# Optimization experiments

Hardware: AMD Instinct MI355X
Metric: run time of the kernel (lower is better)

## Reference

```python
import jax, jax.numpy as jnp
import numpy as np

CHANNEL = 16
KERNEL_SIZE = 5

def _gaussian3d_weight(channel, kernel_size):
    sigma = kernel_size / 6.0
    r = jnp.arange(-(kernel_size // 2), (kernel_size + 1) // 2, dtype=jnp.float32) ** 2
    # sum of squared offsets along each axis -> isotropic Gaussian
    k3 = r[None, None, :] + r[None, :, None] + r[:, None, None]
    k3 = jnp.exp(-k3 / (2.0 * sigma ** 2))
    k3 = k3 / k3.sum()
    # depthwise weight: [C_out=C, C_in/groups=1, kD, kH, kW]
    return jnp.broadcast_to(k3, (channel, 1, kernel_size, kernel_size, kernel_size))

def setup_inputs() -> dict:
    key = jax.random.key(0)
    x = jax.random.normal(key, (2, CHANNEL, 64, 128, 128), dtype=jnp.float32)
    weight = _gaussian3d_weight(CHANNEL, KERNEL_SIZE)
    return {"x": x, "weight": weight}

def reference(x, weight):
    # depthwise Conv3d, padding='same', groups=channel, no bias
    return jax.lax.conv_general_dilated(
        x, weight,
        window_strides=(1, 1, 1),
        padding='SAME',
        dimension_numbers=('NCDHW', 'OIDHW', 'NCDHW'),
        feature_group_count=CHANNEL,
    )
```

## Files before the change

### kernel.cpp

```cpp
#include <hip/hip_runtime.h>


#define DD 64
#define HH 128
#define WW 128
#define TH 8
#define NC 16
#define PITCH 136
#define RAWROWS 12
#define XOFF 4
#define ZCHUNK 32

__global__ __launch_bounds__(256, 4)
void gauss3d_sep_kernel(const float* __restrict__ x,
                        const float* __restrict__ wt,
                        float* __restrict__ out)
{
    __shared__ float raw[RAWROWS][PITCH];
    __shared__ float ybuf[TH][PITCH];
    __shared__ float wlds[16];

    const int tid   = threadIdx.x;
    const int ytile = blockIdx.x;
    const int slab  = blockIdx.y;
    const int z0    = blockIdx.z * ZCHUNK;
    const int by    = ytile * TH;
    const int ch    = slab & (NC - 1);

    const float* xs = x   + (size_t)slab * DD * HH * WW;
    float*       os = out + (size_t)slab * DD * HH * WW;

    for (int i = tid; i < RAWROWS * PITCH; i += 256) (&raw[0][0])[i]  = 0.f;
    for (int i = tid; i < TH * PITCH;      i += 256) (&ybuf[0][0])[i] = 0.f;

    if (tid < 15) {
        const int a = tid / 5, q = tid % 5;
        const float* wp = wt + ch * 125;
        float s = 0.f;
        for (int u = 0; u < 5; ++u)
            for (int v = 0; v < 5; ++v) {
                const int i0 = (a == 0) ? q : u;
                const int j0 = (a == 1) ? q : ((a == 0) ? u : v);
                const int k0 = (a == 2) ? q : v;
                s += wp[i0 * 25 + j0 * 5 + k0];
            }
        wlds[a * 5 + q] = s;
    }
    __syncthreads();

    float wz[5], wy[5], wx[5];
#pragma unroll
    for (int i = 0; i < 5; ++i) { wz[i] = wlds[i]; wy[i] = wlds[5 + i]; wx[i] = wlds[10 + i]; }

    const int ty = tid >> 5;
    const int x0 = (tid & 31) << 2;

    const int  r1  = tid >> 5;
    const int  r2  = r1 + 8;
    const int  gy1 = by + r1 - 2;
    const int  gy2 = by + r2 - 2;
    const bool v1  = (gy1 >= 0) && (gy1 < HH);
    const bool v2  = (gy2 >= 0) && (gy2 < HH);
    const int  cx4 = (tid & 31) << 2;

    float ring[5][4];
#pragma unroll
    for (int i = 0; i < 5; ++i)
#pragma unroll
        for (int j = 0; j < 4; ++j) ring[i][j] = 0.f;

    auto ypass_chunk = [&](int cc) {
        const int row = cc / 34;
        const int col = (cc - row * 34) << 2;
        float4 acc = make_float4(0.f, 0.f, 0.f, 0.f);
#pragma unroll
        for (int dy = 0; dy < 5; ++dy) {
            const float4 rv = *(const float4*)&raw[row + dy][col];
            const float  w  = wy[dy];
            acc.x += w * rv.x; acc.y += w * rv.y;
            acc.z += w * rv.z; acc.w += w * rv.w;
        }
        *(float4*)&ybuf[row][col] = acc;
    };

    for (int zs = z0 - 2; zs < z0 + ZCHUNK + 2; ++zs) {
        float snew[4];
        if (zs >= 0 && zs < DD) {
            const float* sl = xs + (size_t)zs * HH * WW;
            if (v1) *(float4*)&raw[r1][XOFF + cx4] = *(const float4*)(sl + gy1 * WW + cx4);
            if (v2) *(float4*)&raw[r2][XOFF + cx4] = *(const float4*)(sl + gy2 * WW + cx4);
            __syncthreads();
            ypass_chunk(tid);
            if (tid < 16) ypass_chunk(tid + 256);
            __syncthreads();
            const float4 a0 = *(const float4*)&ybuf[ty][x0];
            const float4 a1 = *(const float4*)&ybuf[ty][x0 + 4];
            const float4 a2 = *(const float4*)&ybuf[ty][x0 + 8];
            const float ya[12] = { a0.x, a0.y, a0.z, a0.w,
                                   a1.x, a1.y, a1.z, a1.w,
                                   a2.x, a2.y, a2.z, a2.w };
#pragma unroll
            for (int j = 0; j < 4; ++j) {
                float s = 0.f;
#pragma unroll
                for (int i = 0; i < 5; ++i) s += wx[i] * ya[j + i + 2];
                snew[j] = s;
            }
        } else {
#pragma unroll
            for (int j = 0; j < 4; ++j) snew[j] = 0.f;
        }

#pragma unroll
        for (int i = 0; i < 4; ++i)
#pragma unroll
            for (int j = 0; j < 4; ++j) ring[i][j] = ring[i + 1][j];
#pragma unroll
        for (int j = 0; j < 4; ++j) ring[4][j] = snew[j];

        const int zo = zs - 2;
        if (zo >= z0 && zo < z0 + ZCHUNK) {
            float4 o; o.x = o.y = o.z = o.w = 0.f;
#pragma unroll
            for (int k = 0; k < 5; ++k) {
                o.x += wz[k] * ring[k][0];
                o.y += wz[k] * ring[k][1];
                o.z += wz[k] * ring[k][2];
                o.w += wz[k] * ring[k][3];
            }
            *(float4*)(os + (size_t)zo * HH * WW + (size_t)(by + ty) * WW + x0) = o;
        }
    }
}

extern "C" void kernel_launch(void* const* d_in, const int* in_sizes, int n_in,
                              void* d_out, int out_size, void* d_ws, size_t ws_size,
                              hipStream_t stream)
{
    const float* x = (const float*)d_in[0];
    const float* w = (const float*)d_in[1];
    float*       o = (float*)d_out;

    dim3 grid(HH / TH, 2 * NC, DD / ZCHUNK);
    gauss3d_sep_kernel<<<grid, 256, 0, stream>>>(x, w, o);
}
```

Measured before the change: 259.7 us.

## Replace LDS staging with direct global row loads and lane shuffles for x-pass

```diff
diff --git a/kernel.cpp b/kernel.cpp
--- a/kernel.cpp
+++ b/kernel.cpp
@@ -6,32 +6,26 @@
 #define WW 128
 #define TH 8
 #define NC 16
-#define PITCH 136
-#define RAWROWS 12
-#define XOFF 4
-#define ZCHUNK 32
+#define ZCHUNK 16
+#define SLICE (HH * WW)
 
-__global__ __launch_bounds__(256, 4)
+typedef float f32x4 __attribute__((ext_vector_type(4)));
+
+__global__ __launch_bounds__(256, 8)
 void gauss3d_sep_kernel(const float* __restrict__ x,
                         const float* __restrict__ wt,
                         float* __restrict__ out)
 {
-    __shared__ float raw[RAWROWS][PITCH];
-    __shared__ float ybuf[TH][PITCH];
     __shared__ float wlds[16];
 
-    const int tid   = threadIdx.x;
-    const int ytile = blockIdx.x;
-    const int slab  = blockIdx.y;
-    const int z0    = blockIdx.z * ZCHUNK;
-    const int by    = ytile * TH;
-    const int ch    = slab & (NC - 1);
+    const int tid  = threadIdx.x;
+    const int by   = blockIdx.x * TH;
+    const int slab = blockIdx.y;
+    const int z0   = blockIdx.z * ZCHUNK;
+    const int ch   = slab & (NC - 1);
 
-    const float* xs = x   + (size_t)slab * DD * HH * WW;
-    float*       os = out + (size_t)slab * DD * HH * WW;
-
-    for (int i = tid; i < RAWROWS * PITCH; i += 256) (&raw[0][0])[i]  = 0.f;
-    for (int i = tid; i < TH * PITCH;      i += 256) (&ybuf[0][0])[i] = 0.f;
+    const float* xs = x   + (size_t)slab * DD * SLICE;
+    float*       os = out + (size_t)slab * DD * SLICE;
 
     if (tid < 15) {
         const int a = tid / 5, q = tid % 5;
@@ -48,89 +42,79 @@
     }
     __syncthreads();
 
-    float wz[5], wy[5], wx[5];
+    const int ty     = tid >> 5;
+    const int lane31 = tid & 31;
+    const int x0     = lane31 << 2;
+    const int gy     = by + ty;
+
+    float wzc[5], wxc[5], wyv[5];
+    int   roff[5];
 #pragma unroll
-    for (int i = 0; i < 5; ++i) { wz[i] = wlds[i]; wy[i] = wlds[5 + i]; wx[i] = wlds[10 + i]; }
+    for (int i = 0; i < 5; ++i) {
+        wzc[i] = wlds[i];
+        wxc[i] = wlds[10 + i];
+        const int  r = gy - 2 + i;
+        const bool v = (r >= 0) && (r < HH);
+        wyv[i]  = v ? wlds[5 + i] : 0.f;
+        roff[i] = (v ? r : gy) * WW + x0;
+    }
 
-    const int ty = tid >> 5;
-    const int x0 = (tid & 31) << 2;
+    float4 r0, r1, r2, r3, r4;
+    r0 = r1 = r2 = r3 = r4 = make_float4(0.f, 0.f, 0.f, 0.f);
 
-    const int  r1  = tid >> 5;
-    const int  r2  = r1 + 8;
-    const int  gy1 = by + r1 - 2;
-    const int  gy2 = by + r2 - 2;
-    const bool v1  = (gy1 >= 0) && (gy1 < HH);
-    const bool v2  = (gy2 >= 0) && (gy2 < HH);
-    const int  cx4 = (tid & 31) << 2;
+    const int zbase = z0 - 2;
 
-    float ring[5][4];
-#pragma unroll
-    for (int i = 0; i < 5; ++i)
-#pragma unroll
-        for (int j = 0; j < 4; ++j) ring[i][j] = 0.f;
+#define GSTEP(o0, o1, o2, o3, o4, I)                                         \
+    {                                                                        \
+        const int zs = zbase + (I);                                          \
+        float4 sv = make_float4(0.f, 0.f, 0.f, 0.f);                         \
+        if ((unsigned)zs < (unsigned)DD) {               \
+            const float* sl = xs + (size_t)zs * SLICE;                       \
+            float4 yv = make_float4(0.f, 0.f, 0.f, 0.f);                     \
+            _Pragma("unroll")                                                \
+            for (int dy = 0; dy < 5; ++dy) {                                 \
+                const float4 rv = *(const float4*)(sl + roff[dy]);           \
+                const float  w  = wyv[dy];                                   \
+                yv.x += w * rv.x; yv.y += w * rv.y;                          \
+                yv.z += w * rv.z; yv.w += w * rv.w;                          \
+            }                                                                \
+            float Lz = __shfl(yv.z, tid - 1, 64);                            \
+            float Lw = __shfl(yv.w, tid - 1, 64);                            \
+            float Rx = __shfl(yv.x, tid + 1, 64);                            \
+            float Ry = __shfl(yv.y, tid + 1, 64);                            \
+            if (lane31 == 0)  { Lz = 0.f; Lw = 0.f; }                        \
+            if (lane31 == 31) { Rx = 0.f; Ry = 0.f; }                        \
+            sv.x = wxc[0]*Lz   + wxc[1]*Lw   + wxc[2]*yv.x + wxc[3]*yv.y + wxc[4]*yv.z; \
+            sv.y = wxc[0]*Lw   + wxc[1]*yv.x + wxc[2]*yv.y + wxc[3]*yv.z + wxc[4]*yv.w; \
+            sv.z = wxc[0]*yv.x + wxc[1]*yv.y + wxc[2]*yv.z + wxc[3]*yv.w + wxc[4]*Rx;   \
+            sv.w = wxc[0]*yv.y + wxc[1]*yv.z + wxc[2]*yv.w + wxc[3]*Rx   + wxc[4]*Ry;   \
+        }                                                                    \
+        o4 = sv;                                                             \
+        const int zo = zs - 2;                                               \
+        if (zo >= z0) {                          \
+            f32x4 ov;                                                        \
+            ov.x = wzc[0]*o0.x + wzc[1]*o1.x + wzc[2]*o2.x + wzc[3]*o3.x + wzc[4]*o4.x; \
+            ov.y = wzc[0]*o0.y + wzc[1]*o1.y + wzc[2]*o2.y + wzc[3]*o3.y + wzc[4]*o4.y; \
+            ov.z = wzc[0]*o0.z + wzc[1]*o1.z + wzc[2]*o2.z + wzc[3]*o3.z + wzc[4]*o4.z; \
+            ov.w = wzc[0]*o0.w + wzc[1]*o1.w + wzc[2]*o2.w + wzc[3]*o3.w + wzc[4]*o4.w; \
+            f32x4* dst = (f32x4*)(os + (size_t)zo * SLICE + gy * WW + x0);   \
+            __builtin_nontemporal_store(ov, dst);   \
+        }                                                                    \
+    }
 
-    auto ypass_chunk = [&](int cc) {
-        const int row = cc / 34;
-        const int col = (cc - row * 34) << 2;
-        float4 acc = make_float4(0.f, 0.f, 0.f, 0.f);
-#pragma unroll
-        for (int dy = 0; dy < 5; ++dy) {
-            const float4 rv = *(const float4*)&raw[row + dy][col];
-            const float  w  = wy[dy];
-            acc.x += w * rv.x; acc.y += w * rv.y;
-            acc.z += w * rv.z; acc.w += w * rv.w;
-        }
-        *(float4*)&ybuf[row][col] = acc;
-    };
-
-    for (int zs = z0 - 2; zs < z0 + ZCHUNK + 2; ++zs) {
-        float snew[4];
-        if (zs >= 0 && zs < DD) {
-            const float* sl = xs + (size_t)zs * HH * WW;
-            if (v1) *(float4*)&raw[r1][XOFF + cx4] = *(const float4*)(sl + gy1 * WW + cx4);
-            if (v2) *(float4*)&raw[r2][XOFF + cx4] = *(const float4*)(sl + gy2 * WW + cx4);
-            __syncthreads();
-            ypass_chunk(tid);
-            if (tid < 16) ypass_chunk(tid + 256);
-            __syncthreads();
-            const float4 a0 = *(const float4*)&ybuf[ty][x0];
-            const float4 a1 = *(const float4*)&ybuf[ty][x0 + 4];
-            const float4 a2 = *(const float4*)&ybuf[ty][x0 + 8];
-            const float ya[12] = { a0.x, a0.y, a0.z, a0.w,
-                                   a1.x, a1.y, a1.z, a1.w,
-                                   a2.x, a2.y, a2.z, a2.w };
-#pragma unroll
-            for (int j = 0; j < 4; ++j) {
-                float s = 0.f;
-#pragma unroll
-                for (int i = 0; i < 5; ++i) s += wx[i] * ya[j + i + 2];
-                snew[j] = s;
-            }
-        } else {
-#pragma unroll
-            for (int j = 0; j < 4; ++j) snew[j] = 0.f;
-        }
-
-#pragma unroll
-        for (int i = 0; i < 4; ++i)
-#pragma unroll
-            for (int j = 0; j < 4; ++j) ring[i][j] = ring[i + 1][j];
-#pragma unroll
-        for (int j = 0; j < 4; ++j) ring[4][j] = snew[j];
-
-        const int zo = zs - 2;
-        if (zo >= z0 && zo < z0 + ZCHUNK) {
-            float4 o; o.x = o.y = o.z = o.w = 0.f;
-#pragma unroll
-            for (int k = 0; k < 5; ++k) {
-                o.x += wz[k] * ring[k][0];
-                o.y += wz[k] * ring[k][1];
-                o.z += wz[k] * ring[k][2];
-                o.w += wz[k] * ring[k][3];
-            }
-            *(float4*)(os + (size_t)zo * HH * WW + (size_t)(by + ty) * WW + x0) = o;
-        }
+    GSTEP(r1, r2, r3, r4, r0, 0)
+    GSTEP(r2, r3, r4, r0, r1, 1)
+    GSTEP(r3, r4, r0, r1, r2, 2)
+    GSTEP(r4, r0, r1, r2, r3, 3)
+    GSTEP(r0, r1, r2, r3, r4, 4)
+    for (int g = 5; g < 4 + ZCHUNK; g += 5) {
+        GSTEP(r1, r2, r3, r4, r0, g + 0)
+        GSTEP(r2, r3, r4, r0, r1, g + 1)
+        GSTEP(r3, r4, r0, r1, r2, g + 2)
+        GSTEP(r4, r0, r1, r2, r3, g + 3)
+        GSTEP(r0, r1, r2, r3, r4, g + 4)
     }
+#undef GSTEP
 }
 
 extern "C" void kernel_launch(void* const* d_in, const int* in_sizes, int n_in,
```

Result: slower. 404.0 us (+55.6%).
